# Kernel optimization log

Measured on AMD Instinct MI355X. Metric: run time of the kernel, lower is better.

Reference implementation:

```python
import jax, jax.numpy as jnp
import numpy as np

N = 8192
F_IN = 256
F_OUT = 256


def setup_inputs() -> dict:
    key = jax.random.key(0)
    k1, k2, k3 = jax.random.split(key, 3)
    H = jax.random.normal(k1, (N, F_IN), dtype=jnp.float32)
    A_tilde = jax.random.uniform(k2, (N, N), dtype=jnp.float32)  # positive -> valid degrees
    # xavier_uniform for W: limit = sqrt(6/(fan_in+fan_out))
    limit = np.sqrt(6.0 / (F_IN + F_OUT)).astype(np.float32)
    W = jax.random.uniform(k3, (F_IN, F_OUT), dtype=jnp.float32, minval=-limit, maxval=limit)
    return {"H": H, "A_tilde": A_tilde, "W": W}


def reference(H, A_tilde, W):
    # H(l+1) = relu(D^-1/2 A D^-1/2 H W)
    # Diagonal matmuls expressed as row/col rescaling (same math, O(N^2)).
    d_inv_sqrt = jnp.sum(A_tilde, axis=1) ** -0.5          # [N]
    A_norm = d_inv_sqrt[:, None] * A_tilde * d_inv_sqrt[None, :]  # [N,N]
    H_next = (A_norm @ H) @ W                              # [N,F_out]
    return jax.nn.relu(H_next)
```

## Files before the change

### kernel.cpp

```cpp
#include <hip/hip_runtime.h>
#include <hip/hip_bf16.h>

#define N_ROWS 8192
#define F_DIM  256

typedef __bf16 bf16x8_t __attribute__((ext_vector_type(8)));
typedef float  f32x4_t  __attribute__((ext_vector_type(4)));
typedef float  f32x2_t  __attribute__((ext_vector_type(2)));

static __device__ __forceinline__ unsigned short f2bf(float x) {
    union { __hip_bfloat16 h; unsigned short u; } c;
    c.h = __float2bfloat16(x);
    return c.u;
}
static __device__ __forceinline__ unsigned pk2(float lo, float hi) {
    return (unsigned)f2bf(lo) | ((unsigned)f2bf(hi) << 16);
}

__global__ __launch_bounds__(256) void wconv_kernel(const float* __restrict__ W,
                                                    unsigned short* __restrict__ Ws) {
    const int kb = blockIdx.x;
    const int t  = threadIdx.x;
    __shared__ float wt[32][257];
    const int r = t >> 3, g = t & 7;
    const float* src = W + (kb * 32 + r) * F_DIM + g * 32;
#pragma unroll
    for (int i = 0; i < 8; ++i) {
        float4 v = *(const float4*)(src + i * 4);
        wt[r][g * 32 + i * 4 + 0] = v.x;
        wt[r][g * 32 + i * 4 + 1] = v.y;
        wt[r][g * 32 + i * 4 + 2] = v.z;
        wt[r][g * 32 + i * 4 + 3] = v.w;
    }
    __syncthreads();
    unsigned o[16];
#pragma unroll
    for (int k = 0; k < 32; k += 2) o[k >> 1] = pk2(wt[k][t], wt[k + 1][t]);
    uint4* dst = (uint4*)(Ws + kb * 8192 + t * 32);
#pragma unroll
    for (int i = 0; i < 4; ++i) dst[i] = make_uint4(o[4*i], o[4*i+1], o[4*i+2], o[4*i+3]);
}

__global__ __launch_bounds__(1024) void prep_kernel(const float* __restrict__ A,
                                                    const float* __restrict__ H,
                                                    float* __restrict__ dvec,
                                                    unsigned short* __restrict__ Xs) {
    const int kb = blockIdx.x;
    const int t  = threadIdx.x;
    __shared__ float psum[32][33];
    __shared__ float dl[32];
    __shared__ float ht[32][257];

    const int r = t >> 5, g = t & 31;
    const float* arow = A + (size_t)(kb * 32 + r) * N_ROWS;
    float s0 = 0.f, s1 = 0.f, s2 = 0.f, s3 = 0.f;
#pragma unroll 8
    for (int i = 0; i < 64; ++i) {
        f32x4_t v = __builtin_nontemporal_load((f32x4_t*)(arow + (i * 32 + g) * 4));
        s0 += v.x; s1 += v.y; s2 += v.z; s3 += v.w;
    }
    psum[r][g] = (s0 + s1) + (s2 + s3);
    __syncthreads();
    if (t < 32) {
        float s = 0.f;
#pragma unroll
        for (int i = 0; i < 32; ++i) s += psum[t][i];
        float d = 1.0f / sqrtf(s);
        dl[t] = d;
        dvec[kb * 32 + t] = d;
    }
    __syncthreads();
    {
        const int hr = t >> 5, hg = t & 31;
        const float* hsrc = H + (size_t)(kb * 32 + hr) * F_DIM + hg * 8;
        float4 v0 = ((const float4*)hsrc)[0];
        float4 v1 = ((const float4*)hsrc)[1];
        const float d = dl[hr];
        ht[hr][hg * 8 + 0] = v0.x * d;
        ht[hr][hg * 8 + 1] = v0.y * d;
        ht[hr][hg * 8 + 2] = v0.z * d;
        ht[hr][hg * 8 + 3] = v0.w * d;
        ht[hr][hg * 8 + 4] = v1.x * d;
        ht[hr][hg * 8 + 5] = v1.y * d;
        ht[hr][hg * 8 + 6] = v1.z * d;
        ht[hr][hg * 8 + 7] = v1.w * d;
    }
    __syncthreads();
    const int n = t >> 2, q = t & 3;
    unsigned o[4];
#pragma unroll
    for (int i = 0; i < 4; ++i) {
        int k = q * 8 + i * 2;
        o[i] = pk2(ht[k][n], ht[k + 1][n]);
    }
    *(uint4*)(Xs + kb * 8192 + n * 32 + q * 8) = make_uint4(o[0], o[1], o[2], o[3]);
}

template <int KITERS, int ASTRIDE, bool DSCALE, bool RELU>
__global__ __launch_bounds__(512) void gemm_kernel(const float* __restrict__ Amat,
                                                   const unsigned short* __restrict__ Bs,
                                                   const float* __restrict__ dvec,
                                                   float* __restrict__ out) {
    const int t   = threadIdx.x;
    const int blk = blockIdx.x;
    const int w = t >> 6, l = t & 63;
    const int m = l & 15, q = l >> 4;

    __shared__ __align__(16) unsigned short Al[2][1024];

    const int ar = t >> 4, ac = (t & 15) * 2;
    const float* aptr = Amat + (size_t)(blk * 32 + ar) * ASTRIDE + ac;
    const int wr_idx = (ac >> 3) * 256 + (ar >> 4) * 128 + (ar & 15) * 8 + (ac & 7);

    const unsigned short* bptr = Bs + (w * 32 + m) * 32 + q * 8;

    f32x4_t acc[2][2] = {};

    f32x2_t a_cur[2]; uint4 b_cur[2][2];
#pragma unroll
    for (int s = 0; s < 2; ++s) {
        a_cur[s]    = __builtin_nontemporal_load((f32x2_t*)(aptr + s * 32));
        b_cur[s][0] = *(const uint4*)(bptr + s * 8192);
        b_cur[s][1] = *(const uint4*)(bptr + s * 8192 + 512);
    }

    for (int i = 0; i < KITERS; ++i) {
        f32x2_t a_nxt[2]; uint4 b_nxt[2][2];
        if (i + 1 < KITERS) {
            const float* ap = aptr + (i + 1) * 64;
            const unsigned short* bp = bptr + (size_t)(i + 1) * 16384;
#pragma unroll
            for (int s = 0; s < 2; ++s) {
                a_nxt[s]    = __builtin_nontemporal_load((f32x2_t*)(ap + s * 32));
                b_nxt[s][0] = *(const uint4*)(bp + s * 8192);
                b_nxt[s][1] = *(const uint4*)(bp + s * 8192 + 512);
            }
        }
        const unsigned aw0 = pk2(a_cur[0].x, a_cur[0].y);
        const unsigned aw1 = pk2(a_cur[1].x, a_cur[1].y);
        __syncthreads();
        *(unsigned*)&Al[0][wr_idx] = aw0;
        *(unsigned*)&Al[1][wr_idx] = aw1;
        __syncthreads();
#pragma unroll
        for (int s = 0; s < 2; ++s) {
            bf16x8_t af0 = *(const bf16x8_t*)&Al[s][q * 256 + m * 8];
            bf16x8_t af1 = *(const bf16x8_t*)&Al[s][q * 256 + 128 + m * 8];
            bf16x8_t bf0 = __builtin_bit_cast(bf16x8_t, b_cur[s][0]);
            bf16x8_t bf1 = __builtin_bit_cast(bf16x8_t, b_cur[s][1]);
            acc[0][0] = __builtin_amdgcn_mfma_f32_16x16x32_bf16(af0, bf0, acc[0][0], 0, 0, 0);
            acc[0][1] = __builtin_amdgcn_mfma_f32_16x16x32_bf16(af0, bf1, acc[0][1], 0, 0, 0);
            acc[1][0] = __builtin_amdgcn_mfma_f32_16x16x32_bf16(af1, bf0, acc[1][0], 0, 0, 0);
            acc[1][1] = __builtin_amdgcn_mfma_f32_16x16x32_bf16(af1, bf1, acc[1][1], 0, 0, 0);
        }
#pragma unroll
        for (int s = 0; s < 2; ++s) {
            a_cur[s]    = a_nxt[s];
            b_cur[s][0] = b_nxt[s][0];
            b_cur[s][1] = b_nxt[s][1];
        }
    }

    const int gcol0 = w * 32 + m;
#pragma unroll
    for (int mt = 0; mt < 2; ++mt) {
#pragma unroll
        for (int r = 0; r < 4; ++r) {
            const int grow = blk * 32 + mt * 16 + q * 4 + r;
            float ds = 1.0f;
            if (DSCALE) ds = dvec[grow];
#pragma unroll
            for (int nt = 0; nt < 2; ++nt) {
                float v = acc[mt][nt][r] * ds;
                if (RELU) v = fmaxf(v, 0.f);
                out[(size_t)grow * F_DIM + gcol0 + nt * 16] = v;
            }
        }
    }
}

extern "C" void kernel_launch(void* const* d_in, const int* in_sizes, int n_in,
                              void* d_out, int out_size, void* d_ws, size_t ws_size,
                              hipStream_t stream) {
    (void)in_sizes; (void)n_in; (void)out_size; (void)ws_size;
    const float* H = (const float*)d_in[0];
    const float* A = (const float*)d_in[1];
    const float* W = (const float*)d_in[2];
    float* out = (float*)d_out;

    char* ws = (char*)d_ws;
    float*          dvec = (float*)ws;
    unsigned short* Xs   = (unsigned short*)(ws + (32 << 10));
    unsigned short* Wsz  = (unsigned short*)(ws + (32 << 10) + (4 << 20));
    float*          Y    = (float*)(ws + (32 << 10) + (4 << 20) + (128 << 10));

    wconv_kernel<<<dim3(8),   dim3(256),  0, stream>>>(W, Wsz);
    prep_kernel <<<dim3(256), dim3(1024), 0, stream>>>(A, H, dvec, Xs);
    gemm_kernel<128, 8192, true,  false><<<dim3(256), dim3(512), 0, stream>>>(A, Xs, dvec, Y);
    gemm_kernel<4,   256,  false, true ><<<dim3(256), dim3(512), 0, stream>>>(Y, Wsz, nullptr, out);
}
```

Baseline: 465.7 us.

## Load A fragments directly into registers per wave, dropping LDS staging and barriers

The GEMM kernel now has each wave load its own A-operand fragments from global memory as float4 vectors. It converts them to bf16 in registers and feeds them straight to MFMA, replacing the cooperative load into shared memory. This removes two __syncthreads and the LDS round trip per K iteration. The cost is that all eight waves in a block read the same A tile, which multiplies cache traffic, and the loads are no longer nontemporal. Launch bounds also request two blocks per CU.

```diff
diff --git a/kernel.cpp b/kernel.cpp
--- a/kernel.cpp
+++ b/kernel.cpp
@@ -6,7 +6,6 @@
 
 typedef __bf16 bf16x8_t __attribute__((ext_vector_type(8)));
 typedef float  f32x4_t  __attribute__((ext_vector_type(4)));
-typedef float  f32x2_t  __attribute__((ext_vector_type(2)));
 
 static __device__ __forceinline__ unsigned short f2bf(float x) {
     union { __hip_bfloat16 h; unsigned short u; } c;
@@ -15,6 +14,14 @@
 }
 static __device__ __forceinline__ unsigned pk2(float lo, float hi) {
     return (unsigned)f2bf(lo) | ((unsigned)f2bf(hi) << 16);
+}
+static __device__ __forceinline__ bf16x8_t cvt8(f32x4_t lo, f32x4_t hi) {
+    union { unsigned u[4]; bf16x8_t v; } r;
+    r.u[0] = pk2(lo[0], lo[1]);
+    r.u[1] = pk2(lo[2], lo[3]);
+    r.u[2] = pk2(hi[0], hi[1]);
+    r.u[3] = pk2(hi[2], hi[3]);
+    return r.v;
 }
 
 __global__ __launch_bounds__(256) void wconv_kernel(const float* __restrict__ W,
@@ -97,55 +104,54 @@
 }
 
 template <int KITERS, int ASTRIDE, bool DSCALE, bool RELU>
-__global__ __launch_bounds__(512) void gemm_kernel(const float* __restrict__ Amat,
-                                                   const unsigned short* __restrict__ Bs,
-                                                   const float* __restrict__ dvec,
-                                                   float* __restrict__ out) {
+__global__ __launch_bounds__(512, 2) void gemm_kernel(const float* __restrict__ Amat,
+                                                      const unsigned short* __restrict__ Bs,
+                                                      const float* __restrict__ dvec,
+                                                      float* __restrict__ out) {
     const int t   = threadIdx.x;
     const int blk = blockIdx.x;
     const int w = t >> 6, l = t & 63;
     const int m = l & 15, q = l >> 4;
 
-    __shared__ __align__(16) unsigned short Al[2][1024];
-
-    const int ar = t >> 4, ac = (t & 15) * 2;
-    const float* aptr = Amat + (size_t)(blk * 32 + ar) * ASTRIDE + ac;
-    const int wr_idx = (ac >> 3) * 256 + (ar >> 4) * 128 + (ar & 15) * 8 + (ac & 7);
+    const float* a0 = Amat + (size_t)(blk * 32 + m) * ASTRIDE + q * 8;
+    const float* a1 = a0 + (size_t)16 * ASTRIDE;
 
     const unsigned short* bptr = Bs + (w * 32 + m) * 32 + q * 8;
 
     f32x4_t acc[2][2] = {};
 
-    f32x2_t a_cur[2]; uint4 b_cur[2][2];
+    f32x4_t a_cur[2][2][2];
+    uint4   b_cur[2][2];
 #pragma unroll
     for (int s = 0; s < 2; ++s) {
-        a_cur[s]    = __builtin_nontemporal_load((f32x2_t*)(aptr + s * 32));
+        a_cur[s][0][0] = *(const f32x4_t*)(a0 + s * 32);
+        a_cur[s][0][1] = *(const f32x4_t*)(a0 + s * 32 + 4);
+        a_cur[s][1][0] = *(const f32x4_t*)(a1 + s * 32);
+        a_cur[s][1][1] = *(const f32x4_t*)(a1 + s * 32 + 4);
         b_cur[s][0] = *(const uint4*)(bptr + s * 8192);
         b_cur[s][1] = *(const uint4*)(bptr + s * 8192 + 512);
     }
 
     for (int i = 0; i < KITERS; ++i) {
-        f32x2_t a_nxt[2]; uint4 b_nxt[2][2];
+        f32x4_t a_nxt[2][2][2]; uint4 b_nxt[2][2];
         if (i + 1 < KITERS) {
-            const float* ap = aptr + (i + 1) * 64;
+            const float* ap0 = a0 + (i + 1) * 64;
+            const float* ap1 = a1 + (i + 1) * 64;
             const unsigned short* bp = bptr + (size_t)(i + 1) * 16384;
 #pragma unroll
             for (int s = 0; s < 2; ++s) {
-                a_nxt[s]    = __builtin_nontemporal_load((f32x2_t*)(ap + s * 32));
+                a_nxt[s][0][0] = *(const f32x4_t*)(ap0 + s * 32);
+                a_nxt[s][0][1] = *(const f32x4_t*)(ap0 + s * 32 + 4);
+                a_nxt[s][1][0] = *(const f32x4_t*)(ap1 + s * 32);
+                a_nxt[s][1][1] = *(const f32x4_t*)(ap1 + s * 32 + 4);
                 b_nxt[s][0] = *(const uint4*)(bp + s * 8192);
                 b_nxt[s][1] = *(const uint4*)(bp + s * 8192 + 512);
             }
         }
-        const unsigned aw0 = pk2(a_cur[0].x, a_cur[0].y);
-        const unsigned aw1 = pk2(a_cur[1].x, a_cur[1].y);
-        __syncthreads();
-        *(unsigned*)&Al[0][wr_idx] = aw0;
-        *(unsigned*)&Al[1][wr_idx] = aw1;
-        __syncthreads();
 #pragma unroll
         for (int s = 0; s < 2; ++s) {
-            bf16x8_t af0 = *(const bf16x8_t*)&Al[s][q * 256 + m * 8];
-            bf16x8_t af1 = *(const bf16x8_t*)&Al[s][q * 256 + 128 + m * 8];
+            bf16x8_t af0 = cvt8(a_cur[s][0][0], a_cur[s][0][1]);
+            bf16x8_t af1 = cvt8(a_cur[s][1][0], a_cur[s][1][1]);
             bf16x8_t bf0 = __builtin_bit_cast(bf16x8_t, b_cur[s][0]);
             bf16x8_t bf1 = __builtin_bit_cast(bf16x8_t, b_cur[s][1]);
             acc[0][0] = __builtin_amdgcn_mfma_f32_16x16x32_bf16(af0, bf0, acc[0][0], 0, 0, 0);
@@ -155,7 +161,10 @@
         }
 #pragma unroll
         for (int s = 0; s < 2; ++s) {
-            a_cur[s]    = a_nxt[s];
+            a_cur[s][0][0] = a_nxt[s][0][0];
+            a_cur[s][0][1] = a_nxt[s][0][1];
+            a_cur[s][1][0] = a_nxt[s][1][0];
+            a_cur[s][1][1] = a_nxt[s][1][1];
             b_cur[s][0] = b_nxt[s][0];
             b_cur[s][1] = b_nxt[s][1];
         }
```

Result: slower. 642.9 us (+38.0%).

## Split the big GEMM's K range across two blocks and rotate start offsets

Applied to the files above, without the earlier changes.

The A·X GEMM is split along K into two halves, each run by its own block row (grid 256x2). Each block writes a separate partial output Y1 or Y2, and the second GEMM adds the two partials while loading its A operand. Each block also starts its K loop at a rotated offset, and the row-sum pass in prep gets a per-row rotation too, so concurrent blocks hit different memory regions. The aim is to double the number of blocks so the GPU's CUs fill up, and to spread out DRAM and channel traffic. In exchange it writes and reads an extra 8 MB partial buffer.

```diff
diff --git a/kernel.cpp b/kernel.cpp
--- a/kernel.cpp
+++ b/kernel.cpp
@@ -52,11 +52,13 @@
     __shared__ float ht[32][257];
 
     const int r = t >> 5, g = t & 31;
+    const int rot = (kb * 32 + r) & 63;
     const float* arow = A + (size_t)(kb * 32 + r) * N_ROWS;
     float s0 = 0.f, s1 = 0.f, s2 = 0.f, s3 = 0.f;
 #pragma unroll 8
     for (int i = 0; i < 64; ++i) {
-        f32x4_t v = __builtin_nontemporal_load((f32x4_t*)(arow + (i * 32 + g) * 4));
+        const int ii = (i + rot) & 63;
+        f32x4_t v = __builtin_nontemporal_load((f32x4_t*)(arow + (ii * 32 + g) * 4));
         s0 += v.x; s1 += v.y; s2 += v.z; s3 += v.w;
     }
     psum[r][g] = (s0 + s1) + (s2 + s3);
@@ -96,48 +98,68 @@
     *(uint4*)(Xs + kb * 8192 + n * 32 + q * 8) = make_uint4(o[0], o[1], o[2], o[3]);
 }
 
-template <int KITERS, int ASTRIDE, bool DSCALE, bool RELU>
+template <int KITERS, int ASTRIDE, bool DSCALE, bool RELU, bool SUM2, bool ROT>
 __global__ __launch_bounds__(512) void gemm_kernel(const float* __restrict__ Amat,
+                                                   const float* __restrict__ Amat2,
                                                    const unsigned short* __restrict__ Bs,
                                                    const float* __restrict__ dvec,
                                                    float* __restrict__ out) {
-    const int t   = threadIdx.x;
-    const int blk = blockIdx.x;
+    const int t    = threadIdx.x;
+    const int blk  = blockIdx.x;
+    const int half = blockIdx.y;
     const int w = t >> 6, l = t & 63;
     const int m = l & 15, q = l >> 4;
 
     __shared__ __align__(16) unsigned short Al[2][1024];
 
     const int ar = t >> 4, ac = (t & 15) * 2;
-    const float* aptr = Amat + (size_t)(blk * 32 + ar) * ASTRIDE + ac;
+    const float* aptr  = Amat + (size_t)(blk * 32 + ar) * ASTRIDE + ac;
+    const float* aptr2 = SUM2 ? (Amat2 + (size_t)(blk * 32 + ar) * ASTRIDE + ac) : nullptr;
     const int wr_idx = (ac >> 3) * 256 + (ar >> 4) * 128 + (ar & 15) * 8 + (ac & 7);
 
     const unsigned short* bptr = Bs + (w * 32 + m) * 32 + q * 8;
 
+    const int i0    = ROT ? (((blk * 2 + half) * 37) & (KITERS - 1)) : 0;
+    const int kbase = half * KITERS;
+
     f32x4_t acc[2][2] = {};
 
     f32x2_t a_cur[2]; uint4 b_cur[2][2];
-#pragma unroll
-    for (int s = 0; s < 2; ++s) {
-        a_cur[s]    = __builtin_nontemporal_load((f32x2_t*)(aptr + s * 32));
-        b_cur[s][0] = *(const uint4*)(bptr + s * 8192);
-        b_cur[s][1] = *(const uint4*)(bptr + s * 8192 + 512);
-    }
-
-    for (int i = 0; i < KITERS; ++i) {
+    {
+        const int kk = kbase + i0;
+        const float* ap = aptr + (size_t)kk * 64;
+        const unsigned short* bp = bptr + (size_t)kk * 16384;
+#pragma unroll
+        for (int s = 0; s < 2; ++s) {
+            a_cur[s] = __builtin_nontemporal_load((f32x2_t*)(ap + s * 32));
+            if (SUM2) {
+                f32x2_t a2 = __builtin_nontemporal_load((f32x2_t*)(aptr2 + (size_t)kk * 64 + s * 32));
+                a_cur[s] += a2;
+            }
+            b_cur[s][0] = *(const uint4*)(bp + s * 8192);
+            b_cur[s][1] = *(const uint4*)(bp + s * 8192 + 512);
+        }
+    }
+
+    for (int j = 0; j < KITERS; ++j) {
         f32x2_t a_nxt[2]; uint4 b_nxt[2][2];
-        if (i + 1 < KITERS) {
-            const float* ap = aptr + (i + 1) * 64;
-            const unsigned short* bp = bptr + (size_t)(i + 1) * 16384;
+        if (j + 1 < KITERS) {
+            const int kk = kbase + ((i0 + j + 1) & (KITERS - 1));
+            const float* ap = aptr + (size_t)kk * 64;
+            const unsigned short* bp = bptr + (size_t)kk * 16384;
 #pragma unroll
             for (int s = 0; s < 2; ++s) {
-                a_nxt[s]    = __builtin_nontemporal_load((f32x2_t*)(ap + s * 32));
+                a_nxt[s] = __builtin_nontemporal_load((f32x2_t*)(ap + s * 32));
+                if (SUM2) {
+                    f32x2_t a2 = __builtin_nontemporal_load((f32x2_t*)(aptr2 + (size_t)kk * 64 + s * 32));
+                    a_nxt[s] += a2;
+                }
                 b_nxt[s][0] = *(const uint4*)(bp + s * 8192);
                 b_nxt[s][1] = *(const uint4*)(bp + s * 8192 + 512);
             }
         }
-        const unsigned aw0 = pk2(a_cur[0].x, a_cur[0].y);
-        const unsigned aw1 = pk2(a_cur[1].x, a_cur[1].y);
+        const unsigned aw0 = pk2(a_cur[0][0], a_cur[0][1]);
+        const unsigned aw1 = pk2(a_cur[1][0], a_cur[1][1]);
         __syncthreads();
         *(unsigned*)&Al[0][wr_idx] = aw0;
         *(unsigned*)&Al[1][wr_idx] = aw1;
@@ -161,6 +183,7 @@
         }
     }
 
+    float* obase = out + (size_t)half * ((size_t)N_ROWS * F_DIM);
     const int gcol0 = w * 32 + m;
 #pragma unroll
     for (int mt = 0; mt < 2; ++mt) {
@@ -173,7 +196,7 @@
             for (int nt = 0; nt < 2; ++nt) {
                 float v = acc[mt][nt][r] * ds;
                 if (RELU) v = fmaxf(v, 0.f);
-                out[(size_t)grow * F_DIM + gcol0 + nt * 16] = v;
+                obase[(size_t)grow * F_DIM + gcol0 + nt * 16] = v;
             }
         }
     }
@@ -192,10 +215,11 @@
     float*          dvec = (float*)ws;
     unsigned short* Xs   = (unsigned short*)(ws + (32 << 10));
     unsigned short* Wsz  = (unsigned short*)(ws + (32 << 10) + (4 << 20));
-    float*          Y    = (float*)(ws + (32 << 10) + (4 << 20) + (128 << 10));
+    float*          Y1   = (float*)(ws + (32 << 10) + (4 << 20) + (128 << 10));
+    float*          Y2   = Y1 + (size_t)N_ROWS * F_DIM;
 
     wconv_kernel<<<dim3(8),   dim3(256),  0, stream>>>(W, Wsz);
     prep_kernel <<<dim3(256), dim3(1024), 0, stream>>>(A, H, dvec, Xs);
-    gemm_kernel<128, 8192, true,  false><<<dim3(256), dim3(512), 0, stream>>>(A, Xs, dvec, Y);
-    gemm_kernel<4,   256,  false, true ><<<dim3(256), dim3(512), 0, stream>>>(Y, Wsz, nullptr, out);
-}
+    gemm_kernel<64, 8192, true,  false, false, true ><<<dim3(256, 2), dim3(512), 0, stream>>>(A, nullptr, Xs, dvec, Y1);
+    gemm_kernel<4,   256,  false, true,  true,  false><<<dim3(256, 1), dim3(512), 0, stream>>>(Y1, Y2, Wsz, nullptr, out);
+}
```

New measurement: 457.0 us. About the same (-1.9%).

## Pre-convert A to bf16 MFMA layout during rowsum pass; split-K big GEMM

Applied to the files above, without the earlier changes.

The row-sum pass now also writes A as bf16 in a tiled layout that matches the MFMA fragment order. The big GEMM can then load fragments straight from global memory without LDS staging or per-iteration conversion. The big GEMM is split into two K halves across blockIdx.y to double the block count, and the second GEMM sums the two partial results. This adds a 128MB bf16 write of A and an extra 8MB partial buffer, but halves the bytes the main GEMM reads and removes its shared-memory syncs.

```diff
diff --git a/kernel.cpp b/kernel.cpp
--- a/kernel.cpp
+++ b/kernel.cpp
@@ -41,66 +41,148 @@
     for (int i = 0; i < 4; ++i) dst[i] = make_uint4(o[4*i], o[4*i+1], o[4*i+2], o[4*i+3]);
 }
 
-__global__ __launch_bounds__(1024) void prep_kernel(const float* __restrict__ A,
+__global__ __launch_bounds__(256) void pass1_kernel(const float* __restrict__ A,
+                                                    float* __restrict__ rowsum,
+                                                    unsigned short* __restrict__ As) {
+    const int r    = (int)((blockIdx.x * 256 + threadIdx.x) >> 6);
+    const int lane = threadIdx.x & 63;
+    const float* src = A + ((size_t)r << 13) + lane * 8;
+    const int m = r & 15, mt = (r >> 4) & 1;
+    unsigned short* tbase = As + (size_t)(r >> 5) * (128 * 2048) + mt * 128 + m * 8;
+
+    f32x4_t acc0 = {0.f, 0.f, 0.f, 0.f}, acc1 = {0.f, 0.f, 0.f, 0.f};
+#pragma unroll 4
+    for (int it = 0; it < 16; ++it) {
+        const int c0 = it * 512 + lane * 8;
+        f32x4_t v0 = __builtin_nontemporal_load((f32x4_t*)(src + it * 512));
+        f32x4_t v1 = __builtin_nontemporal_load((f32x4_t*)(src + it * 512 + 4));
+        acc0 += v0; acc1 += v1;
+        uint4 pkd;
+        pkd.x = pk2(v0[0], v0[1]); pkd.y = pk2(v0[2], v0[3]);
+        pkd.z = pk2(v1[0], v1[1]); pkd.w = pk2(v1[2], v1[3]);
+        const size_t soff = (size_t)(c0 >> 6) * 2048
+                          + (size_t)((c0 >> 5) & 1) * 1024
+                          + (size_t)((c0 >> 3) & 3) * 256;
+        *(uint4*)(tbase + soff) = pkd;
+    }
+    f32x4_t a = acc0 + acc1;
+    float s = (a[0] + a[1]) + (a[2] + a[3]);
+#pragma unroll
+    for (int off = 1; off < 64; off <<= 1) s += __shfl_xor(s, off);
+    if (lane == 0) rowsum[r] = s;
+}
+
+__global__ __launch_bounds__(256) void prep2_kernel(const float* __restrict__ rowsum,
                                                     const float* __restrict__ H,
                                                     float* __restrict__ dvec,
                                                     unsigned short* __restrict__ Xs) {
     const int kb = blockIdx.x;
     const int t  = threadIdx.x;
-    __shared__ float psum[32][33];
     __shared__ float dl[32];
     __shared__ float ht[32][257];
-
-    const int r = t >> 5, g = t & 31;
-    const float* arow = A + (size_t)(kb * 32 + r) * N_ROWS;
-    float s0 = 0.f, s1 = 0.f, s2 = 0.f, s3 = 0.f;
-#pragma unroll 8
-    for (int i = 0; i < 64; ++i) {
-        f32x4_t v = __builtin_nontemporal_load((f32x4_t*)(arow + (i * 32 + g) * 4));
-        s0 += v.x; s1 += v.y; s2 += v.z; s3 += v.w;
-    }
-    psum[r][g] = (s0 + s1) + (s2 + s3);
-    __syncthreads();
     if (t < 32) {
-        float s = 0.f;
-#pragma unroll
-        for (int i = 0; i < 32; ++i) s += psum[t][i];
-        float d = 1.0f / sqrtf(s);
+        float d = 1.0f / sqrtf(rowsum[kb * 32 + t]);
         dl[t] = d;
         dvec[kb * 32 + t] = d;
     }
     __syncthreads();
-    {
-        const int hr = t >> 5, hg = t & 31;
-        const float* hsrc = H + (size_t)(kb * 32 + hr) * F_DIM + hg * 8;
-        float4 v0 = ((const float4*)hsrc)[0];
-        float4 v1 = ((const float4*)hsrc)[1];
-        const float d = dl[hr];
-        ht[hr][hg * 8 + 0] = v0.x * d;
-        ht[hr][hg * 8 + 1] = v0.y * d;
-        ht[hr][hg * 8 + 2] = v0.z * d;
-        ht[hr][hg * 8 + 3] = v0.w * d;
-        ht[hr][hg * 8 + 4] = v1.x * d;
-        ht[hr][hg * 8 + 5] = v1.y * d;
-        ht[hr][hg * 8 + 6] = v1.z * d;
-        ht[hr][hg * 8 + 7] = v1.w * d;
+    const int hr = t >> 3, hg = t & 7;
+    const float* hsrc = H + (size_t)(kb * 32 + hr) * F_DIM + hg * 32;
+    const float d = dl[hr];
+#pragma unroll
+    for (int i = 0; i < 8; ++i) {
+        float4 v = *(const float4*)(hsrc + i * 4);
+        ht[hr][hg * 32 + i * 4 + 0] = v.x * d;
+        ht[hr][hg * 32 + i * 4 + 1] = v.y * d;
+        ht[hr][hg * 32 + i * 4 + 2] = v.z * d;
+        ht[hr][hg * 32 + i * 4 + 3] = v.w * d;
     }
     __syncthreads();
-    const int n = t >> 2, q = t & 3;
-    unsigned o[4];
-#pragma unroll
-    for (int i = 0; i < 4; ++i) {
-        int k = q * 8 + i * 2;
-        o[i] = pk2(ht[k][n], ht[k + 1][n]);
-    }
-    *(uint4*)(Xs + kb * 8192 + n * 32 + q * 8) = make_uint4(o[0], o[1], o[2], o[3]);
-}
-
-template <int KITERS, int ASTRIDE, bool DSCALE, bool RELU>
-__global__ __launch_bounds__(512) void gemm_kernel(const float* __restrict__ Amat,
-                                                   const unsigned short* __restrict__ Bs,
-                                                   const float* __restrict__ dvec,
-                                                   float* __restrict__ out) {
+    unsigned o[16];
+#pragma unroll
+    for (int k = 0; k < 32; k += 2) o[k >> 1] = pk2(ht[k][t], ht[k + 1][t]);
+    uint4* dst = (uint4*)(Xs + kb * 8192 + t * 32);
+#pragma unroll
+    for (int i = 0; i < 4; ++i) dst[i] = make_uint4(o[4*i], o[4*i+1], o[4*i+2], o[4*i+3]);
+}
+
+template <int KITERS>
+__global__ __launch_bounds__(512) void gemm1_kernel(const unsigned short* __restrict__ As,
+                                                    const unsigned short* __restrict__ Bs,
+                                                    const float* __restrict__ dvec,
+                                                    float* __restrict__ Y) {
+    const int t    = threadIdx.x;
+    const int blk  = blockIdx.x;
+    const int half = blockIdx.y;
+    const int w = t >> 6, l = t & 63;
+    const int m = l & 15, q = l >> 4;
+
+    const unsigned short* ap = As + ((size_t)blk * 128 + (size_t)half * KITERS) * 2048
+                                  + q * 256 + m * 8;
+    const unsigned short* bp = Bs + (size_t)half * KITERS * 16384 + (w * 32 + m) * 32 + q * 8;
+
+    f32x4_t acc[2][2] = {};
+
+    uint4 a_cur[4], b_cur[4];
+    a_cur[0] = *(const uint4*)(ap);
+    a_cur[1] = *(const uint4*)(ap + 128);
+    a_cur[2] = *(const uint4*)(ap + 1024);
+    a_cur[3] = *(const uint4*)(ap + 1152);
+    b_cur[0] = *(const uint4*)(bp);
+    b_cur[1] = *(const uint4*)(bp + 512);
+    b_cur[2] = *(const uint4*)(bp + 8192);
+    b_cur[3] = *(const uint4*)(bp + 8704);
+
+    for (int i = 0; i < KITERS; ++i) {
+        uint4 a_nxt[4], b_nxt[4];
+        if (i + 1 < KITERS) {
+            const unsigned short* an = ap + (size_t)(i + 1) * 2048;
+            const unsigned short* bn = bp + (size_t)(i + 1) * 16384;
+            a_nxt[0] = *(const uint4*)(an);
+            a_nxt[1] = *(const uint4*)(an + 128);
+            a_nxt[2] = *(const uint4*)(an + 1024);
+            a_nxt[3] = *(const uint4*)(an + 1152);
+            b_nxt[0] = *(const uint4*)(bn);
+            b_nxt[1] = *(const uint4*)(bn + 512);
+            b_nxt[2] = *(const uint4*)(bn + 8192);
+            b_nxt[3] = *(const uint4*)(bn + 8704);
+        }
+#pragma unroll
+        for (int s = 0; s < 2; ++s) {
+            bf16x8_t af0 = __builtin_bit_cast(bf16x8_t, a_cur[s * 2 + 0]);
+            bf16x8_t af1 = __builtin_bit_cast(bf16x8_t, a_cur[s * 2 + 1]);
+            bf16x8_t bf0 = __builtin_bit_cast(bf16x8_t, b_cur[s * 2 + 0]);
+            bf16x8_t bf1 = __builtin_bit_cast(bf16x8_t, b_cur[s * 2 + 1]);
+            acc[0][0] = __builtin_amdgcn_mfma_f32_16x16x32_bf16(af0, bf0, acc[0][0], 0, 0, 0);
+            acc[0][1] = __builtin_amdgcn_mfma_f32_16x16x32_bf16(af0, bf1, acc[0][1], 0, 0, 0);
+            acc[1][0] = __builtin_amdgcn_mfma_f32_16x16x32_bf16(af1, bf0, acc[1][0], 0, 0, 0);
+            acc[1][1] = __builtin_amdgcn_mfma_f32_16x16x32_bf16(af1, bf1, acc[1][1], 0, 0, 0);
+        }
+#pragma unroll
+        for (int k = 0; k < 4; ++k) { a_cur[k] = a_nxt[k]; b_cur[k] = b_nxt[k]; }
+    }
+
+    float* obase = Y + (size_t)half * ((size_t)N_ROWS * F_DIM);
+    const int gcol0 = w * 32 + m;
+#pragma unroll
+    for (int mt = 0; mt < 2; ++mt) {
+#pragma unroll
+        for (int r = 0; r < 4; ++r) {
+            const int grow = blk * 32 + mt * 16 + q * 4 + r;
+            const float ds = dvec[grow];
+#pragma unroll
+            for (int nt = 0; nt < 2; ++nt) {
+                obase[(size_t)grow * F_DIM + gcol0 + nt * 16] = acc[mt][nt][r] * ds;
+            }
+        }
+    }
+}
+
+template <int KITERS, int ASTRIDE>
+__global__ __launch_bounds__(512) void gemm2_kernel(const float* __restrict__ Amat,
+                                                    const float* __restrict__ Amat2,
+                                                    const unsigned short* __restrict__ Bs,
+                                                    float* __restrict__ out) {
     const int t   = threadIdx.x;
     const int blk = blockIdx.x;
     const int w = t >> 6, l = t & 63;
@@ -109,7 +191,8 @@
     __shared__ __align__(16) unsigned short Al[2][1024];
 
     const int ar = t >> 4, ac = (t & 15) * 2;
-    const float* aptr = Amat + (size_t)(blk * 32 + ar) * ASTRIDE + ac;
+    const float* aptr  = Amat  + (size_t)(blk * 32 + ar) * ASTRIDE + ac;
+    const float* aptr2 = Amat2 + (size_t)(blk * 32 + ar) * ASTRIDE + ac;
     const int wr_idx = (ac >> 3) * 256 + (ar >> 4) * 128 + (ar & 15) * 8 + (ac & 7);
 
     const unsigned short* bptr = Bs + (w * 32 + m) * 32 + q * 8;
@@ -119,7 +202,9 @@
     f32x2_t a_cur[2]; uint4 b_cur[2][2];
 #pragma unroll
     for (int s = 0; s < 2; ++s) {
-        a_cur[s]    = __builtin_nontemporal_load((f32x2_t*)(aptr + s * 32));
+        f32x2_t a1 = *(const f32x2_t*)(aptr + s * 32);
+        f32x2_t a2 = *(const f32x2_t*)(aptr2 + s * 32);
+        a_cur[s] = a1 + a2;
         b_cur[s][0] = *(const uint4*)(bptr + s * 8192);
         b_cur[s][1] = *(const uint4*)(bptr + s * 8192 + 512);
     }
@@ -127,17 +212,20 @@
     for (int i = 0; i < KITERS; ++i) {
         f32x2_t a_nxt[2]; uint4 b_nxt[2][2];
         if (i + 1 < KITERS) {
-            const float* ap = aptr + (i + 1) * 64;
+            const float* ap  = aptr  + (i + 1) * 64;
+            const float* ap2 = aptr2 + (i + 1) * 64;
             const unsigned short* bp = bptr + (size_t)(i + 1) * 16384;
 #pragma unroll
             for (int s = 0; s < 2; ++s) {
-                a_nxt[s]    = __builtin_nontemporal_load((f32x2_t*)(ap + s * 32));
+                f32x2_t a1 = *(const f32x2_t*)(ap + s * 32);
+                f32x2_t a2 = *(const f32x2_t*)(ap2 + s * 32);
+                a_nxt[s] = a1 + a2;
                 b_nxt[s][0] = *(const uint4*)(bp + s * 8192);
                 b_nxt[s][1] = *(const uint4*)(bp + s * 8192 + 512);
             }
         }
-        const unsigned aw0 = pk2(a_cur[0].x, a_cur[0].y);
-        const unsigned aw1 = pk2(a_cur[1].x, a_cur[1].y);
+        const unsigned aw0 = pk2(a_cur[0][0], a_cur[0][1]);
+        const unsigned aw1 = pk2(a_cur[1][0], a_cur[1][1]);
         __syncthreads();
         *(unsigned*)&Al[0][wr_idx] = aw0;
         *(unsigned*)&Al[1][wr_idx] = aw1;
@@ -167,13 +255,9 @@
 #pragma unroll
         for (int r = 0; r < 4; ++r) {
             const int grow = blk * 32 + mt * 16 + q * 4 + r;
-            float ds = 1.0f;
-            if (DSCALE) ds = dvec[grow];
 #pragma unroll
             for (int nt = 0; nt < 2; ++nt) {
-                float v = acc[mt][nt][r] * ds;
-                if (RELU) v = fmaxf(v, 0.f);
-                out[(size_t)grow * F_DIM + gcol0 + nt * 16] = v;
+                out[(size_t)grow * F_DIM + gcol0 + nt * 16] = fmaxf(acc[mt][nt][r], 0.f);
             }
         }
     }
@@ -189,13 +273,17 @@
     float* out = (float*)d_out;
 
     char* ws = (char*)d_ws;
-    float*          dvec = (float*)ws;
-    unsigned short* Xs   = (unsigned short*)(ws + (32 << 10));
-    unsigned short* Wsz  = (unsigned short*)(ws + (32 << 10) + (4 << 20));
-    float*          Y    = (float*)(ws + (32 << 10) + (4 << 20) + (128 << 10));
-
-    wconv_kernel<<<dim3(8),   dim3(256),  0, stream>>>(W, Wsz);
-    prep_kernel <<<dim3(256), dim3(1024), 0, stream>>>(A, H, dvec, Xs);
-    gemm_kernel<128, 8192, true,  false><<<dim3(256), dim3(512), 0, stream>>>(A, Xs, dvec, Y);
-    gemm_kernel<4,   256,  false, true ><<<dim3(256), dim3(512), 0, stream>>>(Y, Wsz, nullptr, out);
-}
+    float*          dvec   = (float*)ws;
+    float*          rowsum = (float*)(ws + (32 << 10));
+    unsigned short* Wsz    = (unsigned short*)(ws + (64 << 10));
+    unsigned short* Xs     = (unsigned short*)(ws + (256 << 10));
+    float*          Y1     = (float*)(ws + (8 << 20));
+    float*          Y2     = Y1 + (size_t)N_ROWS * F_DIM;
+    unsigned short* As     = (unsigned short*)(ws + (32 << 20));
+
+    wconv_kernel<<<dim3(8),    dim3(256), 0, stream>>>(W, Wsz);
+    pass1_kernel<<<dim3(2048), dim3(256), 0, stream>>>(A, rowsum, As);
+    prep2_kernel<<<dim3(256),  dim3(256), 0, stream>>>(rowsum, H, dvec, Xs);
+    gemm1_kernel<64><<<dim3(256, 2), dim3(512), 0, stream>>>(As, Xs, dvec, Y1);
+    gemm2_kernel<4, 256><<<dim3(256), dim3(512), 0, stream>>>(Y1, Y2, Wsz, out);
+}
```

New measurement: 515.9 us. 1.11x slower.
